# Kernel optimization log

Measured on AMD Instinct MI355X. Metric: run time of the kernel, lower is better.

The kernel has to match this reference:

```python
import jax, jax.numpy as jnp
import numpy as np

K = 5          # kernel size (hard-coded in feature_propogate)
DIL = 2        # dilation
PAD = (K + (DIL - 1) * (K - 1)) // 2  # = 4, same-padding for unfold


def _unfold_w_center(x):
    """torch F.unfold(kernel=5, dilation=2, padding=4) reshaped to [B,C,25,H,W].
    Neighbor index n is kernel row-major (ki*5+kj), matching torch unfold."""
    B, C, H, W = x.shape
    p = jnp.pad(x, ((0, 0), (0, 0), (PAD, PAD), (PAD, PAD)))
    nb = jnp.stack(
        [p[:, :, DIL * i: DIL * i + H, DIL * j: DIL * j + W]
         for i in range(K) for j in range(K)],
        axis=2,
    )  # [B, C, 25, H, W]
    return nb


def setup_inputs() -> dict:
    key = jax.random.key(0)
    k1, k2 = jax.random.split(key)
    feat = jax.random.normal(k1, (4, 128, 128, 128), dtype=jnp.float32) * 0.1
    w_cls = jax.random.normal(k2, (1, 128), dtype=jnp.float32) * 0.1
    b_cls = jnp.zeros((1,), dtype=jnp.float32)
    return {"feat": feat, "w_cls": w_cls, "b_cls": b_cls}


def reference(feat, w_cls, b_cls):
    # feature_propogate: unfold-based local self-attention over 5x5 dilated nbhd
    nb = _unfold_w_center(feat)                          # [B,C,25,H,W]
    corr = jnp.einsum('bchw,bcnhw->bhwn', feat, nb)      # correlation
    attn = jax.nn.softmax(jnp.maximum(corr, 0.0), -1)    # clamp(min=0) + softmax
    prop = jnp.einsum('bcnhw,bhwn->bchw', nb, attn)      # weighted gather-sum
    # 1x1 classifier (Conv2d(C, num_classes, 1))
    logits = jnp.einsum('bchw,oc->bohw', prop, w_cls) + b_cls[None, :, None, None]
    return logits
```

## Files before the change

kernel.cpp:

```cpp
#include <hip/hip_runtime.h>

#define C 128
#define H 128
#define W 128
#define HW (H*W)

__global__ __launch_bounds__(640, 6) void corr_kernel(
    const float* __restrict__ feat, const float* __restrict__ wc,
    float* __restrict__ corrG, float* __restrict__ gG)
{
    __shared__ float corr_s[2][25][W];
    __shared__ float g_s[2][W];

    const int blk0 = blockIdx.x;
    const int blk  = (blk0 & 7) * 64 + (blk0 >> 3);
    const int half = blk & 1;
    const int kp   = (blk >> 1) & 1;
    const int par  = (blk >> 2) & 1;
    const int t    = (blk >> 3) & 15;
    const int b    = blk >> 7;
    const int rb   = 8 * t + par + 4 * kp;

    const int tid  = threadIdx.x;
    const int wv   = tid >> 6;
    const int ti   = wv >> 1;
    const int q    = wv & 1;
    const int lane = tid & 63;
    const int s    = lane >> 5;
    const int pg   = lane & 31;
    const int w0   = pg * 4;

    int sb[3];
#pragma unroll
    for (int u = 0; u < 3; ++u) {
        const int cs = w0 - 4 + 4 * u;
        sb[u] = cs < 0 ? 0 : (cs > W - 4 ? W - 4 : cs);
    }
    const int cbase = half * 64 + q * 32 + s * 16;
    const bool isCtr = (ti == 2);

#pragma unroll 1
    for (int kk = 0; kk < 2; ++kk) {
        const int  r   = rb + 2 * kk;
        const int  rt  = r - 4 + 2 * ti;
        const bool rok = (unsigned)rt < (unsigned)H;

        float acc[5][4];
        float ga[4] = {0.f, 0.f, 0.f, 0.f};
#pragma unroll
        for (int j = 0; j < 5; ++j)
#pragma unroll
            for (int p = 0; p < 4; ++p) acc[j][p] = 0.f;

        if (rok) {
            const float* tp = feat + ((size_t)(b * C + cbase) * H + rt) * W;
            const float* cp = feat + ((size_t)(b * C + cbase) * H + r ) * W + w0;
#pragma unroll 2
            for (int c = 0; c < 16; ++c) {
                const float4 A  = *(const float4*)(tp + sb[0]);
                const float4 Bv = *(const float4*)(tp + sb[1]);
                const float4 Cv = *(const float4*)(tp + sb[2]);
                float4 D;
                if (isCtr) D = Bv;
                else       D = *(const float4*)cp;
                const float wcv = wc[cbase + c];
                const float win[12] = {A.x, A.y, A.z, A.w,
                                       Bv.x, Bv.y, Bv.z, Bv.w,
                                       Cv.x, Cv.y, Cv.z, Cv.w};
                const float ctr[4] = {D.x, D.y, D.z, D.w};
                if (isCtr) {
#pragma unroll
                    for (int p = 0; p < 4; ++p)
                        ga[p] = fmaf(wcv, win[4 + p], ga[p]);
                }
#pragma unroll
                for (int j = 0; j < 5; ++j)
#pragma unroll
                    for (int p = 0; p < 4; ++p)
                        acc[j][p] = fmaf(ctr[p], win[p + 2 * j], acc[j][p]);
                tp += HW; cp += HW;
            }
        }

#pragma unroll
        for (int j = 0; j < 5; ++j)
#pragma unroll
            for (int p = 0; p < 4; ++p)
                acc[j][p] += __shfl_xor(acc[j][p], 32);
        if (isCtr) {
#pragma unroll
            for (int p = 0; p < 4; ++p) ga[p] += __shfl_xor(ga[p], 32);
        }

        if (s == 0) {
#pragma unroll
            for (int j = 0; j < 5; ++j)
#pragma unroll
                for (int p = 0; p < 4; ++p) {
                    const int  col = w0 + p - 4 + 2 * j;
                    const bool ok  = rok && ((unsigned)col < (unsigned)W);
                    corr_s[q][ti * 5 + j][w0 + p] = ok ? acc[j][p] : 0.f;
                }
            if (isCtr) {
#pragma unroll
                for (int p = 0; p < 4; ++p) g_s[q][w0 + p] = ga[p];
            }
        }
        __syncthreads();

        float* cg = corrG + (size_t)((b * H + r) * 2 + half) * (25 * W);
        const float* s0 = &corr_s[0][0][0];
        const float* s1 = &corr_s[1][0][0];
        for (int idx = tid; idx < 25 * W; idx += 640)
            cg[idx] = s0[idx] + s1[idx];
        if (tid < W)
            gG[(size_t)((b * H + r) * 2 + half) * W + tid] = g_s[0][tid] + g_s[1][tid];
        __syncthreads();
    }
}

__global__ __launch_bounds__(128) void soft_kernel(
    const float* __restrict__ corrG, const float* __restrict__ gG,
    const float* __restrict__ bc, float* __restrict__ out)
{
    const int blk0 = blockIdx.x;
    const int xcd  = blk0 & 7;
    const int idx  = blk0 >> 3;
    const int b    = xcd >> 1;
    const int r    = (xcd & 1) * 64 + idx;
    const int w    = threadIdx.x;

    const size_t base = ((size_t)(b * H + r)) * 2;
    const float* c0 = corrG + base * (25 * W);
    const float* c1 = c0 + (25 * W);

    float v[25], m = 0.f;
#pragma unroll
    for (int n = 0; n < 25; ++n) {
        v[n] = fmaxf(c0[n * W + w] + c1[n * W + w], 0.f);
        m = fmaxf(m, v[n]);
    }
    float sum = 0.f, num = 0.f;
#pragma unroll
    for (int i = 0; i < 5; ++i) {
        const int  rt  = r - 4 + 2 * i;
        const bool riv = (unsigned)rt < (unsigned)H;
        const size_t gb = ((size_t)(b * H + (riv ? rt : 0))) * 2 * W;
#pragma unroll
        for (int j = 0; j < 5; ++j) {
            const float e = __expf(v[i * 5 + j] - m);
            sum += e;
            const int  wt = w - 4 + 2 * j;
            const bool ok = riv && ((unsigned)wt < (unsigned)W);
            const int  wi = ok ? wt : 0;
            const float gv = gG[gb + wi] + gG[gb + W + wi];
            num = fmaf(e, ok ? gv : 0.f, num);
        }
    }
    out[((size_t)(b * H + r)) * W + w] = num / sum + bc[0];
}

extern "C" void kernel_launch(void* const* d_in, const int* in_sizes, int n_in,
                              void* d_out, int out_size, void* d_ws, size_t ws_size,
                              hipStream_t stream) {
    const float* feat = (const float*)d_in[0];
    const float* wcls = (const float*)d_in[1];
    const float* bcls = (const float*)d_in[2];
    float* outp  = (float*)d_out;
    float* corrG = (float*)d_ws;
    float* gG    = corrG + (size_t)1024 * 25 * W;

    corr_kernel<<<dim3(512), dim3(640), 0, stream>>>(feat, wcls, corrG, gG);
    soft_kernel<<<dim3(512), dim3(128), 0, stream>>>(corrG, gG, bcls, outp);
}
```

Before: 107.6 us.

## Split corr kernel into small per-(row, tap-row, channel-half) blocks with LDS atomics

The fused 640-thread block, which handled two output rows and all five tap rows, is replaced by 5120 blocks of 128 threads. Each block covers one output row, one tap row and one channel half, and its two waves' partial sums are combined with shared-memory atomicAdd instead of two separate LDS buffers. The soft kernel reads the new [row][tap-row][half][5][W] layout, with block indexing simplified and the XCD swizzle dropped. This is meant to raise occupancy and parallelism, at the cost of more blocks, redundant loads of the centre row across the five tap-row blocks, and LDS atomic contention.

```diff
diff --git a/kernel.cpp b/kernel.cpp
--- a/kernel.cpp
+++ b/kernel.cpp
@@ -5,140 +5,130 @@
 #define W 128
 #define HW (H*W)
 
-__global__ __launch_bounds__(640, 6) void corr_kernel(
+__global__ __launch_bounds__(128, 8) void corr_kernel(
     const float* __restrict__ feat, const float* __restrict__ wc,
     float* __restrict__ corrG, float* __restrict__ gG)
 {
-    __shared__ float corr_s[2][25][W];
-    __shared__ float g_s[2][W];
+    __shared__ float corr_s[5][W];
+    __shared__ float g_s[W];
 
     const int blk0 = blockIdx.x;
-    const int blk  = (blk0 & 7) * 64 + (blk0 >> 3);
+    const int blk  = (blk0 & 7) * 640 + (blk0 >> 3);
     const int half = blk & 1;
-    const int kp   = (blk >> 1) & 1;
-    const int par  = (blk >> 2) & 1;
-    const int t    = (blk >> 3) & 15;
-    const int b    = blk >> 7;
-    const int rb   = 8 * t + par + 4 * kp;
+    const int ti   = (blk >> 1) % 5;
+    const int rr   = blk / 10;
+    const int b    = rr >> 7;
+    const int r    = rr & 127;
 
     const int tid  = threadIdx.x;
     const int wv   = tid >> 6;
-    const int ti   = wv >> 1;
-    const int q    = wv & 1;
     const int lane = tid & 63;
     const int s    = lane >> 5;
     const int pg   = lane & 31;
     const int w0   = pg * 4;
 
-    int sb[3];
-#pragma unroll
-    for (int u = 0; u < 3; ++u) {
-        const int cs = w0 - 4 + 4 * u;
-        sb[u] = cs < 0 ? 0 : (cs > W - 4 ? W - 4 : cs);
-    }
-    const int cbase = half * 64 + q * 32 + s * 16;
+    for (int i = tid; i < 5 * W; i += 128) (&corr_s[0][0])[i] = 0.f;
+    if (tid < W) g_s[tid] = 0.f;
+    __syncthreads();
+
+    const int  rt    = r - 4 + 2 * ti;
+    const bool rok   = (unsigned)rt < (unsigned)H;
     const bool isCtr = (ti == 2);
 
-#pragma unroll 1
-    for (int kk = 0; kk < 2; ++kk) {
-        const int  r   = rb + 2 * kk;
-        const int  rt  = r - 4 + 2 * ti;
-        const bool rok = (unsigned)rt < (unsigned)H;
+    float acc[5][4];
+    float ga[4] = {0.f, 0.f, 0.f, 0.f};
+#pragma unroll
+    for (int j = 0; j < 5; ++j)
+#pragma unroll
+        for (int p = 0; p < 4; ++p) acc[j][p] = 0.f;
 
-        float acc[5][4];
-        float ga[4] = {0.f, 0.f, 0.f, 0.f};
+    if (rok) {
+        int sb[3];
+#pragma unroll
+        for (int u = 0; u < 3; ++u) {
+            const int cs = w0 - 4 + 4 * u;
+            sb[u] = cs < 0 ? 0 : (cs > W - 4 ? W - 4 : cs);
+        }
+        const int cbase = half * 64 + wv * 32 + s * 16;
+        const float* tp = feat + ((size_t)(b * C + cbase) * H + rt) * W;
+        const float* cp = feat + ((size_t)(b * C + cbase) * H + r ) * W + w0;
+#pragma unroll 2
+        for (int c = 0; c < 16; ++c) {
+            const float4 A  = *(const float4*)(tp + sb[0]);
+            const float4 Bv = *(const float4*)(tp + sb[1]);
+            const float4 Cv = *(const float4*)(tp + sb[2]);
+            float4 D;
+            if (isCtr) D = Bv;
+            else       D = *(const float4*)cp;
+            const float wcv = wc[cbase + c];
+            const float win[12] = {A.x, A.y, A.z, A.w,
+                                   Bv.x, Bv.y, Bv.z, Bv.w,
+                                   Cv.x, Cv.y, Cv.z, Cv.w};
+            const float ctr[4] = {D.x, D.y, D.z, D.w};
+            if (isCtr) {
+#pragma unroll
+                for (int p = 0; p < 4; ++p)
+                    ga[p] = fmaf(wcv, win[4 + p], ga[p]);
+            }
+#pragma unroll
+            for (int j = 0; j < 5; ++j)
+#pragma unroll
+                for (int p = 0; p < 4; ++p)
+                    acc[j][p] = fmaf(ctr[p], win[p + 2 * j], acc[j][p]);
+            tp += HW; cp += HW;
+        }
+    }
+
+#pragma unroll
+    for (int j = 0; j < 5; ++j)
+#pragma unroll
+        for (int p = 0; p < 4; ++p)
+            acc[j][p] += __shfl_xor(acc[j][p], 32);
+    if (isCtr) {
+#pragma unroll
+        for (int p = 0; p < 4; ++p) ga[p] += __shfl_xor(ga[p], 32);
+    }
+
+    if (s == 0) {
 #pragma unroll
         for (int j = 0; j < 5; ++j)
 #pragma unroll
-            for (int p = 0; p < 4; ++p) acc[j][p] = 0.f;
-
-        if (rok) {
-            const float* tp = feat + ((size_t)(b * C + cbase) * H + rt) * W;
-            const float* cp = feat + ((size_t)(b * C + cbase) * H + r ) * W + w0;
-#pragma unroll 2
-            for (int c = 0; c < 16; ++c) {
-                const float4 A  = *(const float4*)(tp + sb[0]);
-                const float4 Bv = *(const float4*)(tp + sb[1]);
-                const float4 Cv = *(const float4*)(tp + sb[2]);
-                float4 D;
-                if (isCtr) D = Bv;
-                else       D = *(const float4*)cp;
-                const float wcv = wc[cbase + c];
-                const float win[12] = {A.x, A.y, A.z, A.w,
-                                       Bv.x, Bv.y, Bv.z, Bv.w,
-                                       Cv.x, Cv.y, Cv.z, Cv.w};
-                const float ctr[4] = {D.x, D.y, D.z, D.w};
-                if (isCtr) {
-#pragma unroll
-                    for (int p = 0; p < 4; ++p)
-                        ga[p] = fmaf(wcv, win[4 + p], ga[p]);
-                }
-#pragma unroll
-                for (int j = 0; j < 5; ++j)
-#pragma unroll
-                    for (int p = 0; p < 4; ++p)
-                        acc[j][p] = fmaf(ctr[p], win[p + 2 * j], acc[j][p]);
-                tp += HW; cp += HW;
+            for (int p = 0; p < 4; ++p) {
+                const int  col = w0 + p - 4 + 2 * j;
+                const bool ok  = rok && ((unsigned)col < (unsigned)W);
+                if (ok) atomicAdd(&corr_s[j][w0 + p], acc[j][p]);
             }
-        }
-
-#pragma unroll
-        for (int j = 0; j < 5; ++j)
-#pragma unroll
-            for (int p = 0; p < 4; ++p)
-                acc[j][p] += __shfl_xor(acc[j][p], 32);
         if (isCtr) {
 #pragma unroll
-            for (int p = 0; p < 4; ++p) ga[p] += __shfl_xor(ga[p], 32);
+            for (int p = 0; p < 4; ++p) atomicAdd(&g_s[w0 + p], ga[p]);
         }
+    }
+    __syncthreads();
 
-        if (s == 0) {
-#pragma unroll
-            for (int j = 0; j < 5; ++j)
-#pragma unroll
-                for (int p = 0; p < 4; ++p) {
-                    const int  col = w0 + p - 4 + 2 * j;
-                    const bool ok  = rok && ((unsigned)col < (unsigned)W);
-                    corr_s[q][ti * 5 + j][w0 + p] = ok ? acc[j][p] : 0.f;
-                }
-            if (isCtr) {
-#pragma unroll
-                for (int p = 0; p < 4; ++p) g_s[q][w0 + p] = ga[p];
-            }
-        }
-        __syncthreads();
-
-        float* cg = corrG + (size_t)((b * H + r) * 2 + half) * (25 * W);
-        const float* s0 = &corr_s[0][0][0];
-        const float* s1 = &corr_s[1][0][0];
-        for (int idx = tid; idx < 25 * W; idx += 640)
-            cg[idx] = s0[idx] + s1[idx];
-        if (tid < W)
-            gG[(size_t)((b * H + r) * 2 + half) * W + tid] = g_s[0][tid] + g_s[1][tid];
-        __syncthreads();
-    }
+    float* cg = corrG + (size_t)((rr * 5 + ti) * 2 + half) * (5 * W);
+    for (int i = tid; i < 5 * W; i += 128) cg[i] = (&corr_s[0][0])[i];
+    if (isCtr && tid < W)
+        gG[(size_t)(rr * 2 + half) * W + tid] = g_s[tid];
 }
 
 __global__ __launch_bounds__(128) void soft_kernel(
     const float* __restrict__ corrG, const float* __restrict__ gG,
     const float* __restrict__ bc, float* __restrict__ out)
 {
-    const int blk0 = blockIdx.x;
-    const int xcd  = blk0 & 7;
-    const int idx  = blk0 >> 3;
-    const int b    = xcd >> 1;
-    const int r    = (xcd & 1) * 64 + idx;
-    const int w    = threadIdx.x;
-
-    const size_t base = ((size_t)(b * H + r)) * 2;
-    const float* c0 = corrG + base * (25 * W);
-    const float* c1 = c0 + (25 * W);
+    const int rr = blockIdx.x;
+    const int b  = rr >> 7;
+    const int r  = rr & 127;
+    const int w  = threadIdx.x;
 
     float v[25], m = 0.f;
 #pragma unroll
-    for (int n = 0; n < 25; ++n) {
-        v[n] = fmaxf(c0[n * W + w] + c1[n * W + w], 0.f);
-        m = fmaxf(m, v[n]);
+    for (int i = 0; i < 5; ++i) {
+        const float* c0 = corrG + (size_t)((rr * 5 + i) * 2) * (5 * W);
+#pragma unroll
+        for (int j = 0; j < 5; ++j) {
+            v[i * 5 + j] = fmaxf(c0[j * W + w] + c0[5 * W + j * W + w], 0.f);
+            m = fmaxf(m, v[i * 5 + j]);
+        }
     }
     float sum = 0.f, num = 0.f;
 #pragma unroll
@@ -157,7 +147,7 @@
             num = fmaf(e, ok ? gv : 0.f, num);
         }
     }
-    out[((size_t)(b * H + r)) * W + w] = num / sum + bc[0];
+    out[(size_t)rr * W + w] = num / sum + bc[0];
 }
 
 extern "C" void kernel_launch(void* const* d_in, const int* in_sizes, int n_in,
@@ -168,8 +158,8 @@
     const float* bcls = (const float*)d_in[2];
     float* outp  = (float*)d_out;
     float* corrG = (float*)d_ws;
-    float* gG    = corrG + (size_t)1024 * 25 * W;
+    float* gG    = corrG + (size_t)512 * 5 * 2 * 5 * W;
 
-    corr_kernel<<<dim3(512), dim3(640), 0, stream>>>(feat, wcls, corrG, gG);
+    corr_kernel<<<dim3(5120), dim3(128), 0, stream>>>(feat, wcls, corrG, gG);
     soft_kernel<<<dim3(512), dim3(128), 0, stream>>>(corrG, gG, bcls, outp);
 }
```

Result: slower. 154.9 us (+43.9%).
